# Optimization experiments

Measured on AMD Instinct MI355X. Metric: run time of the kernel, lower is better.

## Reference

```python
import jax, jax.numpy as jnp
import numpy as np


def setup_inputs() -> dict:
    key = jax.random.key(0)
    k1, k2, k3, k4, k5 = jax.random.split(key, 5)
    N = 2048
    H = W = 256
    opacity = jax.random.uniform(k1, (N,), dtype=jnp.float32)
    # means in pixel coordinates, uniformly covering the raster
    means = jax.random.uniform(k2, (N, 2), dtype=jnp.float32) * jnp.array([W, H], jnp.float32)
    # stds in pixels, in [1, 9) so splats cover multiple pixels
    stds = jax.random.uniform(k3, (N, 2), dtype=jnp.float32) * 8.0 + 1.0
    # correlation coefficient in (-0.95, 0.95)
    rhos = (jax.random.uniform(k4, (N,), dtype=jnp.float32) * 2.0 - 1.0) * 0.95
    colors = jax.random.uniform(k5, (N, 3), dtype=jnp.float32)
    return {
        "opacity": opacity,
        "means": means,
        "stds": stds,
        "rhos": rhos,
        "colors": colors,
        "image_height": H,
        "image_width": W,
        "scale_factor": 1,
        "raster_ratio": 3,
    }


def reference(opacity, means, stds, rhos, colors, image_height, image_width, scale_factor, raster_ratio):
    """2D Gaussian splat rasterization.

    Each Gaussian n contributes opacity[n] * exp(-0.5 * d^T Sigma_n^{-1} d) * colors[n]
    to every pixel within raster_ratio standard deviations (Mahalanobis cutoff).
    Sigma_n = [[sx^2, rho*sx*sy], [rho*sx*sy, sy^2]], with stds scaled by scale_factor.
    Output: [H, W, 3] image.
    """
    H, W = image_height, image_width
    sx = stds[:, 0] * scale_factor  # [N]
    sy = stds[:, 1] * scale_factor  # [N]
    rho = rhos
    # inverse covariance entries (per Gaussian)
    one_m_r2 = 1.0 - rho * rho
    inv_a = 1.0 / (sx * sx * one_m_r2)          # Sigma^-1 [0,0]
    inv_c = 1.0 / (sy * sy * one_m_r2)          # Sigma^-1 [1,1]
    inv_b = -rho / (sx * sy * one_m_r2)         # Sigma^-1 [0,1]

    # pixel centers
    xs = jnp.arange(W, dtype=jnp.float32) + 0.5  # [W]
    ys = jnp.arange(H, dtype=jnp.float32) + 0.5  # [H]
    dx = xs[None, None, :] - means[:, 0][:, None, None]  # [N,1,W]
    dy = ys[None, :, None] - means[:, 1][:, None, None]  # [N,H,1]

    # squared Mahalanobis distance, [N,H,W]
    mahal2 = (
        inv_a[:, None, None] * dx * dx
        + 2.0 * inv_b[:, None, None] * dx * dy
        + inv_c[:, None, None] * dy * dy
    )
    cutoff2 = jnp.float32(raster_ratio * raster_ratio)
    weight = jnp.where(mahal2 <= cutoff2, jnp.exp(-0.5 * mahal2), 0.0)  # [N,H,W]
    alpha = opacity[:, None, None] * weight  # [N,H,W]
    # composite: sum over Gaussians
    out = jnp.einsum("nhw,nc->hwc", alpha, colors)  # [H,W,3]
    return out
```

## Files before the change

kernel.cpp:

```cpp
#include <hip/hip_runtime.h>


#define TILE_W 16
#define TILE_H 16
#define CHUNK  1024

__global__ __launch_bounds__(256)
void gsplat_kernel(const float* __restrict__ opacity,
                   const float* __restrict__ means,
                   const float* __restrict__ stds,
                   const float* __restrict__ rhos,
                   const float* __restrict__ colors,
                   const int* __restrict__ hp,
                   const int* __restrict__ wp,
                   const int* __restrict__ sp,
                   const int* __restrict__ rp,
                   float* __restrict__ out,
                   int N)
{
    __shared__ float s_rec[CHUNK * 8];
    __shared__ int s_cnt;

    const int W = wp[0];
    const float scale = (float)sp[0];
    const float ratio = (float)rp[0];
    const float cutoff2 = ratio * ratio;

    const int tiles_x = W / TILE_W;
    const int tile = blockIdx.x;
    const int tx = tile % tiles_x;
    const int ty = tile / tiles_x;

    const int tid = threadIdx.x;
    const int lx = tid & (TILE_W - 1);
    const int ly = tid / TILE_W;
    const int px = tx * TILE_W + lx;
    const int py = ty * TILE_H + ly;
    const float pxc = px + 0.5f;
    const float pyc = py + 0.5f;

    const float tx0 = tx * TILE_W + 0.5f;
    const float tx1 = tx * TILE_W + (TILE_W - 1) + 0.5f;
    const float ty0 = ty * TILE_H + 0.5f;
    const float ty1 = ty * TILE_H + (TILE_H - 1) + 0.5f;

    float accr = 0.0f, accg = 0.0f, accb = 0.0f;

    for (int base = 0; base < N; base += CHUNK) {
        __syncthreads();
        if (tid == 0) s_cnt = 0;
        __syncthreads();

        const int lim = min(N, base + CHUNK);
        for (int g = base + tid; g < lim; g += 256) {
            const float mx = means[2 * g];
            const float my = means[2 * g + 1];
            const float sx = stds[2 * g] * scale;
            const float sy = stds[2 * g + 1] * scale;
            const float ex = ratio * sx;
            const float ey = ratio * sy;
            if (mx - ex <= tx1 && mx + ex >= tx0 &&
                my - ey <= ty1 && my + ey >= ty0) {
                const float rho = rhos[g];
                const float omr = 1.0f - rho * rho;
                const float ia = 1.0f / (sx * sx * omr);
                const float ic = 1.0f / (sy * sy * omr);
                const float ib = -rho / (sx * sy * omr);
                const float op = opacity[g];
                const int idx = atomicAdd(&s_cnt, 1);
                float* r = &s_rec[idx * 8];
                r[0] = mx;
                r[1] = my;
                r[2] = ia;
                r[3] = ib;
                r[4] = ic;
                r[5] = op * colors[3 * g];
                r[6] = op * colors[3 * g + 1];
                r[7] = op * colors[3 * g + 2];
            }
        }
        __syncthreads();

        const int cnt = s_cnt;
        for (int i = 0; i < cnt; ++i) {
            const float* r = &s_rec[i * 8];
            const float dx = pxc - r[0];
            const float dy = pyc - r[1];
            const float m = r[2] * dx * dx + 2.0f * r[3] * dx * dy + r[4] * dy * dy;
            if (m <= cutoff2) {
                const float w = __expf(-0.5f * m);
                accr = fmaf(w, r[5], accr);
                accg = fmaf(w, r[6], accg);
                accb = fmaf(w, r[7], accb);
            }
        }
    }

    const int o = (py * W + px) * 3;
    out[o + 0] = accr;
    out[o + 1] = accg;
    out[o + 2] = accb;
}

extern "C" void kernel_launch(void* const* d_in, const int* in_sizes, int n_in,
                              void* d_out, int out_size, void* d_ws, size_t ws_size,
                              hipStream_t stream) {
    const float* opacity = (const float*)d_in[0];
    const float* means   = (const float*)d_in[1];
    const float* stds    = (const float*)d_in[2];
    const float* rhos    = (const float*)d_in[3];
    const float* colors  = (const float*)d_in[4];
    const int*   hp      = (const int*)d_in[5];
    const int*   wp      = (const int*)d_in[6];
    const int*   sp      = (const int*)d_in[7];
    const int*   rp      = (const int*)d_in[8];
    float* out = (float*)d_out;

    const int N = in_sizes[0];
    const int n_pixels = out_size / 3;
    const int n_tiles = n_pixels / (TILE_W * TILE_H);

    gsplat_kernel<<<n_tiles, 256, 0, stream>>>(opacity, means, stds, rhos, colors,
                                               hp, wp, sp, rp, out, N);
}
```

Before: 83.32 us.

## Split Gaussians across grid y-dimension with partial buffers and separate reduction

Each tile's Gaussian list is now split into slices of up to 256, one per grid row, so every block culls and splats only one slice and writes its partial image to workspace. A second kernel sums the partial images into the output with float4 loads. Shared-memory atomics for compaction are replaced by a wave ballot/popcount prefix. This targets the under-filled grid of 256 blocks on a large GPU, at the cost of writing and re-reading S full partial images and relying on workspace size.

```diff
diff --git a/kernel.cpp b/kernel.cpp
--- a/kernel.cpp
+++ b/kernel.cpp
@@ -1,105 +1,135 @@
 #include <hip/hip_runtime.h>
 
 
-#define TILE_W 16
-#define TILE_H 16
-#define CHUNK  1024
-
 __global__ __launch_bounds__(256)
-void gsplat_kernel(const float* __restrict__ opacity,
-                   const float* __restrict__ means,
-                   const float* __restrict__ stds,
-                   const float* __restrict__ rhos,
-                   const float* __restrict__ colors,
-                   const int* __restrict__ hp,
-                   const int* __restrict__ wp,
-                   const int* __restrict__ sp,
-                   const int* __restrict__ rp,
-                   float* __restrict__ out,
-                   int N)
+void gsplat_splat(const float* __restrict__ opacity,
+                  const float* __restrict__ means,
+                  const float* __restrict__ stds,
+                  const float* __restrict__ rhos,
+                  const float* __restrict__ colors,
+                  const int* __restrict__ wp,
+                  const int* __restrict__ sp,
+                  const int* __restrict__ rp,
+                  float* __restrict__ partial,
+                  int N, int chunk, int sstride)
 {
-    __shared__ float s_rec[CHUNK * 8];
-    __shared__ int s_cnt;
+    __shared__ float s_rec[256 * 8];
+    __shared__ int s_wcnt[4];
 
     const int W = wp[0];
     const float scale = (float)sp[0];
     const float ratio = (float)rp[0];
     const float cutoff2 = ratio * ratio;
 
-    const int tiles_x = W / TILE_W;
+    const int tiles_x = W / 16;
     const int tile = blockIdx.x;
+    const int s = blockIdx.y;
     const int tx = tile % tiles_x;
     const int ty = tile / tiles_x;
 
     const int tid = threadIdx.x;
-    const int lx = tid & (TILE_W - 1);
-    const int ly = tid / TILE_W;
-    const int px = tx * TILE_W + lx;
-    const int py = ty * TILE_H + ly;
+    const int lx = tid & 15;
+    const int ly = tid >> 4;
+    const int px = tx * 16 + lx;
+    const int py = ty * 16 + ly;
     const float pxc = px + 0.5f;
     const float pyc = py + 0.5f;
 
-    const float tx0 = tx * TILE_W + 0.5f;
-    const float tx1 = tx * TILE_W + (TILE_W - 1) + 0.5f;
-    const float ty0 = ty * TILE_H + 0.5f;
-    const float ty1 = ty * TILE_H + (TILE_H - 1) + 0.5f;
+    const float tx0 = tx * 16 + 0.5f;
+    const float tx1 = tx * 16 + 15.5f;
+    const float ty0 = ty * 16 + 0.5f;
+    const float ty1 = ty * 16 + 15.5f;
 
-    float accr = 0.0f, accg = 0.0f, accb = 0.0f;
-
-    for (int base = 0; base < N; base += CHUNK) {
-        __syncthreads();
-        if (tid == 0) s_cnt = 0;
-        __syncthreads();
-
-        const int lim = min(N, base + CHUNK);
-        for (int g = base + tid; g < lim; g += 256) {
-            const float mx = means[2 * g];
-            const float my = means[2 * g + 1];
-            const float sx = stds[2 * g] * scale;
-            const float sy = stds[2 * g + 1] * scale;
-            const float ex = ratio * sx;
-            const float ey = ratio * sy;
-            if (mx - ex <= tx1 && mx + ex >= tx0 &&
-                my - ey <= ty1 && my + ey >= ty0) {
-                const float rho = rhos[g];
-                const float omr = 1.0f - rho * rho;
-                const float ia = 1.0f / (sx * sx * omr);
-                const float ic = 1.0f / (sy * sy * omr);
-                const float ib = -rho / (sx * sy * omr);
-                const float op = opacity[g];
-                const int idx = atomicAdd(&s_cnt, 1);
-                float* r = &s_rec[idx * 8];
-                r[0] = mx;
-                r[1] = my;
-                r[2] = ia;
-                r[3] = ib;
-                r[4] = ic;
-                r[5] = op * colors[3 * g];
-                r[6] = op * colors[3 * g + 1];
-                r[7] = op * colors[3 * g + 2];
-            }
-        }
-        __syncthreads();
-
-        const int cnt = s_cnt;
-        for (int i = 0; i < cnt; ++i) {
-            const float* r = &s_rec[i * 8];
-            const float dx = pxc - r[0];
-            const float dy = pyc - r[1];
-            const float m = r[2] * dx * dx + 2.0f * r[3] * dx * dy + r[4] * dy * dy;
-            if (m <= cutoff2) {
-                const float w = __expf(-0.5f * m);
-                accr = fmaf(w, r[5], accr);
-                accg = fmaf(w, r[6], accg);
-                accb = fmaf(w, r[7], accb);
-            }
+    const int g = s * chunk + tid;
+    bool pred = false;
+    float mx = 0.f, my = 0.f, ia = 0.f, ib = 0.f, ic = 0.f;
+    if (g < N && tid < chunk) {
+        const float2 mm = ((const float2*)means)[g];
+        const float2 ss = ((const float2*)stds)[g];
+        mx = mm.x; my = mm.y;
+        const float sx = ss.x * scale;
+        const float sy = ss.y * scale;
+        const float ex = ratio * sx;
+        const float ey = ratio * sy;
+        pred = (mx - ex <= tx1) & (mx + ex >= tx0) &
+               (my - ey <= ty1) & (my + ey >= ty0);
+        if (pred) {
+            const float rho = rhos[g];
+            const float omr = 1.0f - rho * rho;
+            ia = 1.0f / (sx * sx * omr);
+            ic = 1.0f / (sy * sy * omr);
+            ib = -rho / (sx * sy * omr);
         }
     }
 
-    const int o = (py * W + px) * 3;
-    out[o + 0] = accr;
-    out[o + 1] = accg;
-    out[o + 2] = accb;
+    const unsigned long long bal = __ballot(pred);
+    const int lane = tid & 63;
+    const int wv = tid >> 6;
+    if (lane == 0) s_wcnt[wv] = __popcll(bal);
+    __syncthreads();
+    int base = 0;
+#pragma unroll
+    for (int i = 0; i < 4; ++i)
+        if (i < wv) base += s_wcnt[i];
+    const int cnt = s_wcnt[0] + s_wcnt[1] + s_wcnt[2] + s_wcnt[3];
+    if (pred) {
+        const int idx = base + __popcll(bal & ((1ull << lane) - 1ull));
+        const float op = opacity[g];
+        float* r = &s_rec[idx * 8];
+        r[0] = mx;
+        r[1] = my;
+        r[2] = ia;
+        r[3] = ib;
+        r[4] = ic;
+        r[5] = op * colors[3 * g];
+        r[6] = op * colors[3 * g + 1];
+        r[7] = op * colors[3 * g + 2];
+    }
+    __syncthreads();
+
+    float accr = 0.0f, accg = 0.0f, accb = 0.0f;
+    for (int i = 0; i < cnt; ++i) {
+        const float* r = &s_rec[i * 8];
+        const float dx = pxc - r[0];
+        const float dy = pyc - r[1];
+        const float m = r[2] * dx * dx + 2.0f * r[3] * dx * dy + r[4] * dy * dy;
+        if (m <= cutoff2) {
+            const float w = __expf(-0.5f * m);
+            accr = fmaf(w, r[5], accr);
+            accg = fmaf(w, r[6], accg);
+            accb = fmaf(w, r[7], accb);
+        }
+    }
+
+    float* dst = partial + (size_t)s * sstride + (py * W + px) * 3;
+    dst[0] = accr;
+    dst[1] = accg;
+    dst[2] = accb;
+}
+
+__global__ __launch_bounds__(256)
+void gsplat_reduce(const float* __restrict__ partial,
+                   float* __restrict__ out,
+                   int npix3, int sstride, int S)
+{
+    const int n4 = npix3 >> 2;
+    const int i = blockIdx.x * 256 + threadIdx.x;
+    if (i < n4) {
+        const int s4 = sstride >> 2;
+        const float4* p4 = (const float4*)partial;
+        float4 a = p4[i];
+        for (int s = 1; s < S; ++s) {
+            const float4 b = p4[(size_t)s * s4 + i];
+            a.x += b.x; a.y += b.y; a.z += b.z; a.w += b.w;
+        }
+        ((float4*)out)[i] = a;
+    }
+    if (blockIdx.x == 0 && threadIdx.x < (npix3 & 3)) {
+        const int j = (npix3 & ~3) + threadIdx.x;
+        float a = partial[j];
+        for (int s = 1; s < S; ++s) a += partial[(size_t)s * sstride + j];
+        out[j] = a;
+    }
 }
 
 extern "C" void kernel_launch(void* const* d_in, const int* in_sizes, int n_in,
@@ -110,16 +140,25 @@
     const float* stds    = (const float*)d_in[2];
     const float* rhos    = (const float*)d_in[3];
     const float* colors  = (const float*)d_in[4];
-    const int*   hp      = (const int*)d_in[5];
     const int*   wp      = (const int*)d_in[6];
     const int*   sp      = (const int*)d_in[7];
     const int*   rp      = (const int*)d_in[8];
     float* out = (float*)d_out;
+    float* partial = (float*)d_ws;
 
     const int N = in_sizes[0];
+    const int npix3 = out_size;
     const int n_pixels = out_size / 3;
-    const int n_tiles = n_pixels / (TILE_W * TILE_H);
+    const int n_tiles = n_pixels / 256;
+    const int S = (N + 255) / 256;
+    const int chunk = (N + S - 1) / S;
+    const int sstride = (npix3 + 3) & ~3;
 
-    gsplat_kernel<<<n_tiles, 256, 0, stream>>>(opacity, means, stds, rhos, colors,
-                                               hp, wp, sp, rp, out, N);
+    dim3 grid(n_tiles, S);
+    gsplat_splat<<<grid, 256, 0, stream>>>(opacity, means, stds, rhos, colors,
+                                           wp, sp, rp, partial, N, chunk, sstride);
+
+    const int n4 = npix3 >> 2;
+    const int rblocks = (n4 + 255) / 256;
+    gsplat_reduce<<<rblocks, 256, 0, stream>>>(partial, out, npix3, sstride, S);
 }
```

Measured after the change: 79.35 us. 4.8% less time.
